# Kernel optimization log

Hardware: AMD Instinct MI355X
Metric: run time of the kernel (lower is better)

The kernel has to match this reference:

```python
import jax, jax.numpy as jnp
import numpy as np

# spconv.SparseConv4d(C_in, 16, (1,3,3,3), stride=1, padding=0) on spatial_shape [1000,1000,40]:
# leading kernel dim is size 1, so this is a regular (non-submanifold) 3D sparse conv,
# valid padding -> output spatial shape (998, 998, 38). Implemented as gather-GEMM-scatter:
# input point p contributes feat(p) @ W[k] to output coord p - offset[k] for each of 27 taps.

N = 200000
C_IN = 64
C_OUT = 16
K = 3
OUT_SP = (998, 998, 38)  # 1000-3+1, 1000-3+1, 40-3+1
SENT = OUT_SP[0] * OUT_SP[1] * OUT_SP[2]  # sentinel linear index for invalid taps


def setup_inputs() -> dict:
    key = jax.random.key(0)
    k1, k2, k3, k4, k5, k6 = jax.random.split(key, 6)
    feats = jax.random.normal(k1, (N, C_IN), dtype=jnp.float32)
    x = jax.random.randint(k2, (N,), 0, 1000, dtype=jnp.int32)
    y = jax.random.randint(k3, (N,), 0, 1000, dtype=jnp.int32)
    z = jax.random.randint(k4, (N,), 0, 40, dtype=jnp.int32)
    coords = jnp.stack([jnp.zeros((N,), jnp.int32), x, y, z], axis=1)  # [N,4] (b,x,y,z)
    fan_in = C_IN * K * K * K
    W = jax.random.normal(k5, (K * K * K, C_IN, C_OUT), dtype=jnp.float32) / np.sqrt(fan_in)
    bias = jax.random.normal(k6, (C_OUT,), dtype=jnp.float32) * 0.01
    return {"input": feats, "coords": coords, "W": W, "bias": bias}


def reference(input, coords, W, bias):
    # kernel tap offsets, C-order over (kx,ky,kz) in [0,3)^3 -> [27,3]
    off = jnp.stack(
        jnp.meshgrid(jnp.arange(K), jnp.arange(K), jnp.arange(K), indexing="ij"),
        axis=-1,
    ).reshape(K * K * K, 3).astype(jnp.int32)
    xyz = coords[:, 1:4]                              # [N,3]
    oc = xyz[:, None, :] - off[None, :, :]            # [N,27,3] output coord per tap
    out_sp = jnp.array(OUT_SP, dtype=jnp.int32)
    valid = jnp.all((oc >= 0) & (oc < out_sp), axis=-1)  # [N,27]
    lin = oc[..., 0] * (OUT_SP[1] * OUT_SP[2]) + oc[..., 1] * OUT_SP[2] + oc[..., 2]
    lin = jnp.where(valid, lin, SENT).reshape(-1)     # [N*27]

    # gather-GEMM: per-tap GEMM over all active voxels
    contrib = jnp.einsum("nc,kco->nko", input, W)     # [N,27,16]
    contrib = jnp.where(valid[..., None], contrib, 0.0).reshape(-1, C_OUT)

    NK = N * (K * K * K)
    uniq, inv = jnp.unique(lin, return_inverse=True, size=NK, fill_value=SENT)
    inv = inv.reshape(-1)
    # scatter-add into unique output sites
    out = jax.ops.segment_sum(contrib, inv, num_segments=NK)  # [NK,16]
    cnt = jax.ops.segment_sum(valid.reshape(-1).astype(jnp.int32), inv, num_segments=NK)
    out = out + jnp.where(cnt[:, None] > 0, bias[None, :], 0.0)
    return out, uniq
```

## Files before the change

### kernel.cpp

```cpp
#include <hip/hip_runtime.h>

#define N_PTS   200000
#define CIN     64
#define COUT    16
#define KK      27
#define SXD     998
#define SYD     998
#define SZD     38
#define STRX    (SYD*SZD)
#define SENTV   (SXD*SYD*SZD)
#define NKTOT   (N_PTS*KK)
#define NWORDS  ((SENTV+31)/32)
#define NCHUNK  ((NWORDS+255)/256)
#define NB      16000

typedef float f32x4 __attribute__((ext_vector_type(4)));

template<int S>
__global__ void mark_kernel(const int* __restrict__ coords, unsigned* __restrict__ bm,
                            unsigned* __restrict__ mu, unsigned* __restrict__ hist) {
    int n = blockIdx.x * blockDim.x + threadIdx.x;
    if (n >= N_PTS) return;
    int4 c = ((const int4*)coords)[n];
    int x = c.y, y = c.z, z = c.w;
    if (hist) {
        unsigned key = ((unsigned)x >> 3) * 128u + ((unsigned)y >> 3);
        atomicAdd(&hist[key], 1u);
    }
    int zlo = z - 2; if (zlo < 0) zlo = 0;
    int zhi = z;     if (zhi > SZD - 1) zhi = SZD - 1;
    unsigned nb = (unsigned)(zhi - zlo + 1);
    unsigned mseed = (1u << nb) - 1u;
    #pragma unroll
    for (int dx = 0; dx < 3; dx++) {
        int ox = x - dx;
        if (ox < 0 || ox >= SXD) continue;
        #pragma unroll
        for (int dy = 0; dy < 3; dy++) {
            int oy = y - dy;
            if (oy < 0 || oy >= SYD) continue;
            int lin = ox*STRX + oy*SZD + zlo;
            unsigned w = (unsigned)lin >> 5;
            unsigned b = (unsigned)lin & 31u;
            unsigned lowm = mseed << b;
            unsigned old = atomicOr(&bm[(size_t)w * S], lowm);
            unsigned col = old & lowm;
            if (col) atomicOr(&mu[(size_t)w * S], col);
            if (b + nb > 32u) {
                unsigned highm = mseed >> (32u - b);
                unsigned old2 = atomicOr(&bm[(size_t)(w+1) * S], highm);
                unsigned col2 = old2 & highm;
                if (col2) atomicOr(&mu[(size_t)(w+1) * S], col2);
            }
        }
    }
}

template<int S>
__global__ void chunk_sums_kernel(const unsigned* __restrict__ bm, unsigned* __restrict__ csums) {
    int w = blockIdx.x * 256 + threadIdx.x;
    unsigned c = (w < NWORDS) ? (unsigned)__popc(bm[(size_t)w * S]) : 0u;
    __shared__ unsigned s[256];
    s[threadIdx.x] = c;
    __syncthreads();
    for (int off = 128; off > 0; off >>= 1) {
        if (threadIdx.x < off) s[threadIdx.x] += s[threadIdx.x + off];
        __syncthreads();
    }
    if (threadIdx.x == 0) csums[blockIdx.x] = s[0];
}

__global__ void scan_all_kernel(const unsigned* __restrict__ csums,
                                unsigned* __restrict__ cprefix,
                                unsigned* __restrict__ Uptr,
                                const unsigned* __restrict__ hist,
                                unsigned* __restrict__ bpos,
                                int do_buckets) {
    __shared__ unsigned s[256];
    __shared__ unsigned run_s;
    if (threadIdx.x == 0) run_s = 0;
    __syncthreads();
    for (int base = 0; base < NCHUNK; base += 256) {
        int i = base + threadIdx.x;
        unsigned v = (i < NCHUNK) ? csums[i] : 0u;
        s[threadIdx.x] = v;
        __syncthreads();
        for (int off = 1; off < 256; off <<= 1) {
            unsigned t = (threadIdx.x >= off) ? s[threadIdx.x - off] : 0u;
            __syncthreads();
            s[threadIdx.x] += t;
            __syncthreads();
        }
        unsigned run = run_s;
        if (i < NCHUNK) cprefix[i] = run + s[threadIdx.x] - v;
        unsigned tile_total = s[255];
        __syncthreads();
        if (threadIdx.x == 255) run_s = run + tile_total;
        __syncthreads();
    }
    if (threadIdx.x == 0) Uptr[0] = run_s;
    if (!do_buckets) return;
    __syncthreads();
    if (threadIdx.x == 0) run_s = 0;
    __syncthreads();
    for (int base = 0; base < NB; base += 256) {
        int i = base + threadIdx.x;
        unsigned v = (i < NB) ? hist[i] : 0u;
        s[threadIdx.x] = v;
        __syncthreads();
        for (int off = 1; off < 256; off <<= 1) {
            unsigned t = (threadIdx.x >= off) ? s[threadIdx.x - off] : 0u;
            __syncthreads();
            s[threadIdx.x] += t;
            __syncthreads();
        }
        unsigned run = run_s;
        if (i < NB) bpos[i] = run + s[threadIdx.x] - v;
        unsigned tile_total = s[255];
        __syncthreads();
        if (threadIdx.x == 255) run_s = run + tile_total;
        __syncthreads();
    }
}

template<int S>
__global__ void word_prefix_kernel(const unsigned* __restrict__ bm,
                                   const unsigned* __restrict__ cprefix,
                                   unsigned* __restrict__ wp) {
    int w = blockIdx.x * 256 + threadIdx.x;
    unsigned v = (w < NWORDS) ? (unsigned)__popc(bm[(size_t)w * S]) : 0u;
    __shared__ unsigned s[256];
    s[threadIdx.x] = v;
    __syncthreads();
    for (int off = 1; off < 256; off <<= 1) {
        unsigned t = (threadIdx.x >= off) ? s[threadIdx.x - off] : 0u;
        __syncthreads();
        s[threadIdx.x] += t;
        __syncthreads();
    }
    if (w < NWORDS) wp[(size_t)w * S] = cprefix[blockIdx.x] + s[threadIdx.x] - v;
}

__global__ void pidx_kernel(const int* __restrict__ coords, unsigned* __restrict__ bpos,
                            int4* __restrict__ csorted) {
    int n = blockIdx.x * blockDim.x + threadIdx.x;
    if (n >= N_PTS) return;
    int4 c = ((const int4*)coords)[n];
    unsigned key = ((unsigned)c.y >> 3) * 128u + ((unsigned)c.z >> 3);
    unsigned pos = atomicAdd(&bpos[key], 1u);
    csorted[pos] = make_int4(n, c.y, c.z, c.w);
}

__global__ void fill_out_kernel(float* __restrict__ out, const float* __restrict__ bias,
                                const unsigned* __restrict__ Uptr) {
    unsigned U = Uptr[0];
    unsigned i = blockIdx.x * blockDim.x + threadIdx.x;
    if (i >= (unsigned)NKTOT * 4u) return;
    unsigned row = i >> 2;
    int q = i & 3;
    float4 v;
    if (row < U) v = ((const float4*)bias)[q];
    else         v = make_float4(0.f, 0.f, 0.f, 0.f);
    ((float4*)out)[i] = v;
}

__global__ void fill_uniq_kernel(float* __restrict__ uniq) {
    unsigned i = blockIdx.x * blockDim.x + threadIdx.x;
    if (i < (unsigned)NKTOT) uniq[i] = (float)SENTV;
}

__global__ void tail_kernel(float* __restrict__ out, float* __restrict__ uniq,
                            const unsigned* __restrict__ Uptr) {
    unsigned U = Uptr[0];
    unsigned i = blockIdx.x * blockDim.x + threadIdx.x;
    if (i >= (unsigned)NKTOT || i < U) return;
    f32x4 z4 = {0.f, 0.f, 0.f, 0.f};
    f32x4* dst = (f32x4*)(out + (size_t)i * COUT);
    #pragma unroll
    for (int q = 0; q < 4; q++) __builtin_nontemporal_store(z4, dst + q);
    __builtin_nontemporal_store((float)SENTV, uniq + i);
}

template<int S, bool DO_BIAS>
__global__ void write_uniq_kernel(const unsigned* __restrict__ bm,
                                  const unsigned* __restrict__ mu,
                                  const unsigned* __restrict__ wp,
                                  const unsigned* __restrict__ Uptr,
                                  float* __restrict__ uniq,
                                  float* __restrict__ out,
                                  const float* __restrict__ bias) {
    __shared__ float sbuf[8192];
    unsigned U = Uptr[0];
    int wfirst = blockIdx.x * 256;
    int wnext  = wfirst + 256;
    unsigned r0 = wp[(size_t)wfirst * S];
    unsigned r1 = (wnext < NWORDS) ? wp[(size_t)wnext * S] : U;
    int w = wfirst + threadIdx.x;
    unsigned bits = 0, r = 0, mbits = 0;
    if (w < NWORDS) {
        bits = bm[(size_t)w * S];
        r    = wp[(size_t)w * S];
        if (DO_BIAS) mbits = mu[(size_t)w * S];
    }
    unsigned bb = bits, rr = r;
    while (bb) {
        int b = __ffs(bb) - 1;
        bb &= bb - 1;
        sbuf[rr - r0] = (float)((unsigned)w * 32u + b);
        rr++;
    }
    __syncthreads();
    unsigned span = r1 - r0;
    for (unsigned j = threadIdx.x; j < span; j += 256)
        __builtin_nontemporal_store(sbuf[j], uniq + r0 + j);
    if (DO_BIAS && bits && mbits) {
        f32x4 bv[4];
        #pragma unroll
        for (int q = 0; q < 4; q++) bv[q] = ((const f32x4*)bias)[q];
        bb = bits; rr = r;
        while (bb) {
            int b = __ffs(bb) - 1;
            bb &= bb - 1;
            if ((mbits >> b) & 1u) {
                f32x4* dst = (f32x4*)(out + (size_t)rr * COUT);
                #pragma unroll
                for (int q = 0; q < 4; q++) __builtin_nontemporal_store(bv[q], dst + q);
            }
            rr++;
        }
    }
}

template<int S, bool SORTED>
__launch_bounds__(256)
__global__ void scatter_mm_kernel(const float* __restrict__ feats,
                                  const int4* __restrict__ cpts,
                                  const float* __restrict__ W,
                                  const float* __restrict__ bias,
                                  const unsigned* __restrict__ bm,
                                  const unsigned* __restrict__ mu,
                                  const unsigned* __restrict__ wp,
                                  float* __restrict__ out) {
    int i = blockIdx.x * 256 + threadIdx.x;
    if (i >= N_PTS) return;
    int dx = blockIdx.y;
    int4 cc = cpts[i];
    int n = SORTED ? cc.x : i;
    int x = cc.y, y = cc.z, z = cc.w;
    int ox = x - dx;
    if (ox < 0 || ox >= SXD) return;

    f32x4 f[CIN/4];
    const f32x4* fin4 = (const f32x4*)(feats + (size_t)n * CIN);
    #pragma unroll
    for (int q = 0; q < CIN/4; q++) f[q] = fin4[q];

    f32x4 bv[4];
    #pragma unroll
    for (int q = 0; q < 4; q++) bv[q] = ((const f32x4*)bias)[q];

    #pragma unroll 1
    for (int dy = 0; dy < 3; dy++) {
        int oy = y - dy;
        if (oy < 0 || oy >= SYD) continue;
        int colbase = ox*STRX + oy*SZD;
        #pragma unroll 1
        for (int dz = 0; dz < 3; dz++) {
            int oz = z - dz;
            if (oz < 0 || oz >= SZD) continue;
            int lin = colbase + oz;
            unsigned word = (unsigned)lin >> 5, bit = (unsigned)lin & 31u;
            unsigned rank;
            bool is_multi;
            if constexpr (S == 4) {
                uint4 md = ((const uint4*)bm)[word];
                rank = md.z + (unsigned)__popc(md.x & ((1u << bit) - 1u));
                is_multi = (md.y >> bit) & 1u;
            } else {
                rank = wp[word] + (unsigned)__popc(bm[word] & ((1u << bit) - 1u));
                is_multi = (mu[word] >> bit) & 1u;
            }

            int m = dx*9 + dy*3 + dz;
            const float* wk = W + (size_t)m * CIN * COUT;
            float acc[COUT];
            #pragma unroll
            for (int o = 0; o < COUT; o++) acc[o] = 0.f;
            #pragma unroll
            for (int c4 = 0; c4 < CIN/4; c4++) {
                f32x4 fv = f[c4];
                const float* wrow = wk + c4 * 4 * COUT;
                #pragma unroll
                for (int o = 0; o < COUT; o++) {
                    acc[o] += fv.x * wrow[o] + fv.y * wrow[COUT + o]
                            + fv.z * wrow[2*COUT + o] + fv.w * wrow[3*COUT + o];
                }
            }

            float* dst = out + (size_t)rank * COUT;
            if (!is_multi) {
                #pragma unroll
                for (int q = 0; q < 4; q++) {
                    f32x4 v;
                    v.x = acc[q*4+0] + bv[q].x;
                    v.y = acc[q*4+1] + bv[q].y;
                    v.z = acc[q*4+2] + bv[q].z;
                    v.w = acc[q*4+3] + bv[q].w;
                    ((f32x4*)dst)[q] = v;
                }
            } else {
                #pragma unroll
                for (int o = 0; o < COUT; o++) atomicAdd(dst + o, acc[o]);
            }
        }
    }
}

extern "C" void kernel_launch(void* const* d_in, const int* in_sizes, int n_in,
                              void* d_out, int out_size, void* d_ws, size_t ws_size,
                              hipStream_t stream) {
    const float* feats  = (const float*)d_in[0];
    const int*   coords = (const int*)d_in[1];
    const float* W      = (const float*)d_in[2];
    const float* bias   = (const float*)d_in[3];
    float* out  = (float*)d_out;
    float* uniq = out + (size_t)NKTOT * COUT;

    unsigned* ws = (unsigned*)d_ws;

    size_t o_meta    = 0;
    size_t o_hist    = o_meta + 4 * (size_t)NWORDS;
    size_t o_bpos    = o_hist + NB;
    size_t o_csums   = o_bpos + NB;
    size_t o_cprefix = o_csums + NCHUNK;
    size_t o_Uptr    = o_cprefix + NCHUNK;
    size_t o_csort   = (o_Uptr + 1 + 3) & ~(size_t)3;
    size_t fast_words = o_csort + 4 * (size_t)N_PTS;

    if (ws_size >= fast_words * sizeof(unsigned)) {
        unsigned* meta    = ws + o_meta;
        unsigned* hist    = ws + o_hist;
        unsigned* bpos    = ws + o_bpos;
        unsigned* csums   = ws + o_csums;
        unsigned* cprefix = ws + o_cprefix;
        unsigned* Uptr    = ws + o_Uptr;
        int4*     csorted = (int4*)(ws + o_csort);

        hipMemsetAsync(meta, 0, (4 * (size_t)NWORDS + NB) * sizeof(unsigned), stream);
        mark_kernel<4><<<(N_PTS + 255) / 256, 256, 0, stream>>>(coords, meta, meta + 1, hist);
        chunk_sums_kernel<4><<<NCHUNK, 256, 0, stream>>>(meta, csums);
        scan_all_kernel<<<1, 256, 0, stream>>>(csums, cprefix, Uptr, hist, bpos, 1);
        pidx_kernel<<<(N_PTS + 255) / 256, 256, 0, stream>>>(coords, bpos, csorted);
        word_prefix_kernel<4><<<NCHUNK, 256, 0, stream>>>(meta, cprefix, meta + 2);
        write_uniq_kernel<4, true><<<NCHUNK, 256, 0, stream>>>(
            meta, meta + 1, meta + 2, Uptr, uniq, out, bias);
        tail_kernel<<<(NKTOT + 255) / 256, 256, 0, stream>>>(out, uniq, Uptr);
        scatter_mm_kernel<4, true><<<dim3((N_PTS + 255) / 256, 3), 256, 0, stream>>>(
            feats, csorted, W, bias, meta, meta + 1, meta + 2, out);
    } else {
        unsigned* bitmap  = ws;
        unsigned* wprefix = ws + NWORDS;
        unsigned* csums   = ws + 2 * (size_t)NWORDS;
        unsigned* cprefix = csums + NCHUNK;
        unsigned* Uptr    = cprefix + NCHUNK;

        hipMemsetAsync(bitmap, 0, (size_t)NWORDS * sizeof(unsigned), stream);
        mark_kernel<1><<<(N_PTS + 255) / 256, 256, 0, stream>>>(coords, bitmap, bitmap, nullptr);
        chunk_sums_kernel<1><<<NCHUNK, 256, 0, stream>>>(bitmap, csums);
        scan_all_kernel<<<1, 256, 0, stream>>>(csums, cprefix, Uptr, nullptr, nullptr, 0);
        word_prefix_kernel<1><<<NCHUNK, 256, 0, stream>>>(bitmap, cprefix, wprefix);
        fill_out_kernel<<<(NKTOT * 4 + 255) / 256, 256, 0, stream>>>(out, bias, Uptr);
        fill_uniq_kernel<<<(NKTOT + 255) / 256, 256, 0, stream>>>(uniq);
        write_uniq_kernel<1, false><<<NCHUNK, 256, 0, stream>>>(
            bitmap, bitmap, wprefix, Uptr, uniq, out, bias);
        scatter_mm_kernel<1, false><<<dim3((N_PTS + 255) / 256, 3), 256, 0, stream>>>(
            feats, (const int4*)coords, W, bias, bitmap, bitmap, wprefix, out);
    }
}
```

Before: 1.251 ms.

## Split interleaved metadata into separate arrays and fuse dx taps into one thread

Replaces the stride-4 interleaved bitmap/multi/prefix layout with separate contiguous arrays. Each scatter thread now handles all three dx offsets instead of one per blockIdx.y, preloading the nine column metadata words and computing the ranks of consecutive z voxels as r0+j. Feature loads and coordinate reads are therefore shared across 27 taps, and metadata lookups drop to about nine per point. The two prefix scans now run in parallel across two blocks. The cost is higher register pressure and fewer threads in the scatter kernel, which lowers parallelism.

```diff
diff --git a/kernel.cpp b/kernel.cpp
--- a/kernel.cpp
+++ b/kernel.cpp
@@ -16,7 +16,6 @@
 
 typedef float f32x4 __attribute__((ext_vector_type(4)));
 
-template<int S>
 __global__ void mark_kernel(const int* __restrict__ coords, unsigned* __restrict__ bm,
                             unsigned* __restrict__ mu, unsigned* __restrict__ hist) {
     int n = blockIdx.x * blockDim.x + threadIdx.x;
@@ -43,23 +42,22 @@
             unsigned w = (unsigned)lin >> 5;
             unsigned b = (unsigned)lin & 31u;
             unsigned lowm = mseed << b;
-            unsigned old = atomicOr(&bm[(size_t)w * S], lowm);
+            unsigned old = atomicOr(&bm[w], lowm);
             unsigned col = old & lowm;
-            if (col) atomicOr(&mu[(size_t)w * S], col);
+            if (col) atomicOr(&mu[w], col);
             if (b + nb > 32u) {
                 unsigned highm = mseed >> (32u - b);
-                unsigned old2 = atomicOr(&bm[(size_t)(w+1) * S], highm);
+                unsigned old2 = atomicOr(&bm[w+1], highm);
                 unsigned col2 = old2 & highm;
-                if (col2) atomicOr(&mu[(size_t)(w+1) * S], col2);
+                if (col2) atomicOr(&mu[w+1], col2);
             }
         }
     }
 }
 
-template<int S>
 __global__ void chunk_sums_kernel(const unsigned* __restrict__ bm, unsigned* __restrict__ csums) {
     int w = blockIdx.x * 256 + threadIdx.x;
-    unsigned c = (w < NWORDS) ? (unsigned)__popc(bm[(size_t)w * S]) : 0u;
+    unsigned c = (w < NWORDS) ? (unsigned)__popc(bm[w]) : 0u;
     __shared__ unsigned s[256];
     s[threadIdx.x] = c;
     __syncthreads();
@@ -78,11 +76,15 @@
                                 int do_buckets) {
     __shared__ unsigned s[256];
     __shared__ unsigned run_s;
+    if (blockIdx.x == 1 && !do_buckets) return;
+    const unsigned* src = (blockIdx.x == 0) ? csums : hist;
+    unsigned* dst       = (blockIdx.x == 0) ? cprefix : bpos;
+    int count           = (blockIdx.x == 0) ? NCHUNK : NB;
     if (threadIdx.x == 0) run_s = 0;
     __syncthreads();
-    for (int base = 0; base < NCHUNK; base += 256) {
+    for (int base = 0; base < count; base += 256) {
         int i = base + threadIdx.x;
-        unsigned v = (i < NCHUNK) ? csums[i] : 0u;
+        unsigned v = (i < count) ? src[i] : 0u;
         s[threadIdx.x] = v;
         __syncthreads();
         for (int off = 1; off < 256; off <<= 1) {
@@ -92,43 +94,20 @@
             __syncthreads();
         }
         unsigned run = run_s;
-        if (i < NCHUNK) cprefix[i] = run + s[threadIdx.x] - v;
+        if (i < count) dst[i] = run + s[threadIdx.x] - v;
         unsigned tile_total = s[255];
         __syncthreads();
         if (threadIdx.x == 255) run_s = run + tile_total;
         __syncthreads();
     }
-    if (threadIdx.x == 0) Uptr[0] = run_s;
-    if (!do_buckets) return;
-    __syncthreads();
-    if (threadIdx.x == 0) run_s = 0;
-    __syncthreads();
-    for (int base = 0; base < NB; base += 256) {
-        int i = base + threadIdx.x;
-        unsigned v = (i < NB) ? hist[i] : 0u;
-        s[threadIdx.x] = v;
-        __syncthreads();
-        for (int off = 1; off < 256; off <<= 1) {
-            unsigned t = (threadIdx.x >= off) ? s[threadIdx.x - off] : 0u;
-            __syncthreads();
-            s[threadIdx.x] += t;
-            __syncthreads();
-        }
-        unsigned run = run_s;
-        if (i < NB) bpos[i] = run + s[threadIdx.x] - v;
-        unsigned tile_total = s[255];
-        __syncthreads();
-        if (threadIdx.x == 255) run_s = run + tile_total;
-        __syncthreads();
-    }
-}
-
-template<int S>
+    if (blockIdx.x == 0 && threadIdx.x == 0) Uptr[0] = run_s;
+}
+
 __global__ void word_prefix_kernel(const unsigned* __restrict__ bm,
                                    const unsigned* __restrict__ cprefix,
                                    unsigned* __restrict__ wp) {
     int w = blockIdx.x * 256 + threadIdx.x;
-    unsigned v = (w < NWORDS) ? (unsigned)__popc(bm[(size_t)w * S]) : 0u;
+    unsigned v = (w < NWORDS) ? (unsigned)__popc(bm[w]) : 0u;
     __shared__ unsigned s[256];
     s[threadIdx.x] = v;
     __syncthreads();
@@ -138,7 +117,7 @@
         s[threadIdx.x] += t;
         __syncthreads();
     }
-    if (w < NWORDS) wp[(size_t)w * S] = cprefix[blockIdx.x] + s[threadIdx.x] - v;
+    if (w < NWORDS) wp[w] = cprefix[blockIdx.x] + s[threadIdx.x] - v;
 }
 
 __global__ void pidx_kernel(const int* __restrict__ coords, unsigned* __restrict__ bpos,
@@ -181,7 +160,7 @@
     __builtin_nontemporal_store((float)SENTV, uniq + i);
 }
 
-template<int S, bool DO_BIAS>
+template<bool DO_BIAS>
 __global__ void write_uniq_kernel(const unsigned* __restrict__ bm,
                                   const unsigned* __restrict__ mu,
                                   const unsigned* __restrict__ wp,
@@ -193,14 +172,14 @@
     unsigned U = Uptr[0];
     int wfirst = blockIdx.x * 256;
     int wnext  = wfirst + 256;
-    unsigned r0 = wp[(size_t)wfirst * S];
-    unsigned r1 = (wnext < NWORDS) ? wp[(size_t)wnext * S] : U;
+    unsigned r0 = wp[wfirst];
+    unsigned r1 = (wnext < NWORDS) ? wp[wnext] : U;
     int w = wfirst + threadIdx.x;
     unsigned bits = 0, r = 0, mbits = 0;
     if (w < NWORDS) {
-        bits = bm[(size_t)w * S];
-        r    = wp[(size_t)w * S];
-        if (DO_BIAS) mbits = mu[(size_t)w * S];
+        bits = bm[w];
+        r    = wp[w];
+        if (DO_BIAS) mbits = mu[w];
     }
     unsigned bb = bits, rr = r;
     while (bb) {
@@ -231,7 +210,7 @@
     }
 }
 
-template<int S, bool SORTED>
+template<bool SORTED>
 __launch_bounds__(256)
 __global__ void scatter_mm_kernel(const float* __restrict__ feats,
                                   const int4* __restrict__ cpts,
@@ -243,12 +222,32 @@
                                   float* __restrict__ out) {
     int i = blockIdx.x * 256 + threadIdx.x;
     if (i >= N_PTS) return;
-    int dx = blockIdx.y;
     int4 cc = cpts[i];
     int n = SORTED ? cc.x : i;
     int x = cc.y, y = cc.z, z = cc.w;
-    int ox = x - dx;
-    if (ox < 0 || ox >= SXD) return;
+
+    int zlo = z - 2; if (zlo < 0) zlo = 0;
+
+    unsigned bmv[9], muv[9], mu2v[9], wpv[9], b0v[9];
+    bool valv[9];
+    #pragma unroll
+    for (int dx = 0; dx < 3; dx++) {
+        int ox = x - dx;
+        #pragma unroll
+        for (int dy = 0; dy < 3; dy++) {
+            int k = dx*3 + dy;
+            int oy = y - dy;
+            bool v = (ox >= 0) & (ox < SXD) & (oy >= 0) & (oy < SYD);
+            valv[k] = v;
+            unsigned lin0 = (unsigned)(ox*STRX + oy*SZD + zlo);
+            unsigned w0 = v ? (lin0 >> 5) : 0u;
+            b0v[k] = lin0 & 31u;
+            bmv[k]  = v ? bm[w0] : 0u;
+            muv[k]  = v ? mu[w0] : 0u;
+            mu2v[k] = (v && (lin0 & 31u) >= 30u) ? mu[w0 + 1] : 0u;
+            wpv[k]  = v ? wp[w0] : 0u;
+        }
+    }
 
     f32x4 f[CIN/4];
     const f32x4* fin4 = (const f32x4*)(feats + (size_t)n * CIN);
@@ -260,57 +259,53 @@
     for (int q = 0; q < 4; q++) bv[q] = ((const f32x4*)bias)[q];
 
     #pragma unroll 1
-    for (int dy = 0; dy < 3; dy++) {
-        int oy = y - dy;
-        if (oy < 0 || oy >= SYD) continue;
-        int colbase = ox*STRX + oy*SZD;
+    for (int dx = 0; dx < 3; dx++) {
         #pragma unroll 1
-        for (int dz = 0; dz < 3; dz++) {
-            int oz = z - dz;
-            if (oz < 0 || oz >= SZD) continue;
-            int lin = colbase + oz;
-            unsigned word = (unsigned)lin >> 5, bit = (unsigned)lin & 31u;
-            unsigned rank;
-            bool is_multi;
-            if constexpr (S == 4) {
-                uint4 md = ((const uint4*)bm)[word];
-                rank = md.z + (unsigned)__popc(md.x & ((1u << bit) - 1u));
-                is_multi = (md.y >> bit) & 1u;
-            } else {
-                rank = wp[word] + (unsigned)__popc(bm[word] & ((1u << bit) - 1u));
-                is_multi = (mu[word] >> bit) & 1u;
-            }
-
-            int m = dx*9 + dy*3 + dz;
-            const float* wk = W + (size_t)m * CIN * COUT;
-            float acc[COUT];
+        for (int dy = 0; dy < 3; dy++) {
+            int k = dx*3 + dy;
+            if (!valv[k]) continue;
+            unsigned b0 = b0v[k];
+            unsigned r0 = wpv[k] + (unsigned)__popc(bmv[k] & ((1u << b0) - 1u));
+            unsigned mlo = muv[k], mhi = mu2v[k];
             #pragma unroll
-            for (int o = 0; o < COUT; o++) acc[o] = 0.f;
-            #pragma unroll
-            for (int c4 = 0; c4 < CIN/4; c4++) {
-                f32x4 fv = f[c4];
-                const float* wrow = wk + c4 * 4 * COUT;
+            for (int dz = 0; dz < 3; dz++) {
+                int oz = z - dz;
+                if (oz < 0 || oz >= SZD) continue;
+                unsigned j = (unsigned)(oz - zlo);
+                unsigned bb = b0 + j;
+                bool ismul = (((bb < 32u) ? (mlo >> bb) : (mhi >> (bb - 32u))) & 1u) != 0u;
+                unsigned rank = r0 + j;
+
+                const float* wk = W + (size_t)(dx*9 + dy*3 + dz) * (CIN*COUT);
+                float acc[COUT];
                 #pragma unroll
-                for (int o = 0; o < COUT; o++) {
-                    acc[o] += fv.x * wrow[o] + fv.y * wrow[COUT + o]
-                            + fv.z * wrow[2*COUT + o] + fv.w * wrow[3*COUT + o];
+                for (int o = 0; o < COUT; o++) acc[o] = 0.f;
+                #pragma unroll
+                for (int c4 = 0; c4 < CIN/4; c4++) {
+                    f32x4 fv = f[c4];
+                    const float* wrow = wk + c4 * 4 * COUT;
+                    #pragma unroll
+                    for (int o = 0; o < COUT; o++) {
+                        acc[o] += fv.x * wrow[o] + fv.y * wrow[COUT + o]
+                                + fv.z * wrow[2*COUT + o] + fv.w * wrow[3*COUT + o];
+                    }
                 }
-            }
-
-            float* dst = out + (size_t)rank * COUT;
-            if (!is_multi) {
-                #pragma unroll
-                for (int q = 0; q < 4; q++) {
-                    f32x4 v;
-                    v.x = acc[q*4+0] + bv[q].x;
-                    v.y = acc[q*4+1] + bv[q].y;
-                    v.z = acc[q*4+2] + bv[q].z;
-                    v.w = acc[q*4+3] + bv[q].w;
-                    ((f32x4*)dst)[q] = v;
+
+                float* dst = out + (size_t)rank * COUT;
+                if (!ismul) {
+                    #pragma unroll
+                    for (int q = 0; q < 4; q++) {
+                        f32x4 vv;
+                        vv.x = acc[q*4+0] + bv[q].x;
+                        vv.y = acc[q*4+1] + bv[q].y;
+                        vv.z = acc[q*4+2] + bv[q].z;
+                        vv.w = acc[q*4+3] + bv[q].w;
+                        ((f32x4*)dst)[q] = vv;
+                    }
+                } else {
+                    #pragma unroll
+                    for (int o = 0; o < COUT; o++) atomicAdd(dst + o, acc[o]);
                 }
-            } else {
-                #pragma unroll
-                for (int o = 0; o < COUT; o++) atomicAdd(dst + o, acc[o]);
             }
         }
     }
@@ -328,9 +323,11 @@
 
     unsigned* ws = (unsigned*)d_ws;
 
-    size_t o_meta    = 0;
-    size_t o_hist    = o_meta + 4 * (size_t)NWORDS;
-    size_t o_bpos    = o_hist + NB;
+    size_t o_bm      = 0;
+    size_t o_mu      = o_bm + NWORDS;
+    size_t o_hist    = o_mu + NWORDS;
+    size_t o_wp      = o_hist + NB;
+    size_t o_bpos    = o_wp + NWORDS;
     size_t o_csums   = o_bpos + NB;
     size_t o_cprefix = o_csums + NCHUNK;
     size_t o_Uptr    = o_cprefix + NCHUNK;
@@ -338,42 +335,44 @@
     size_t fast_words = o_csort + 4 * (size_t)N_PTS;
 
     if (ws_size >= fast_words * sizeof(unsigned)) {
-        unsigned* meta    = ws + o_meta;
+        unsigned* bm      = ws + o_bm;
+        unsigned* mu      = ws + o_mu;
         unsigned* hist    = ws + o_hist;
+        unsigned* wp      = ws + o_wp;
         unsigned* bpos    = ws + o_bpos;
         unsigned* csums   = ws + o_csums;
         unsigned* cprefix = ws + o_cprefix;
         unsigned* Uptr    = ws + o_Uptr;
         int4*     csorted = (int4*)(ws + o_csort);
 
-        hipMemsetAsync(meta, 0, (4 * (size_t)NWORDS + NB) * sizeof(unsigned), stream);
-        mark_kernel<4><<<(N_PTS + 255) / 256, 256, 0, stream>>>(coords, meta, meta + 1, hist);
-        chunk_sums_kernel<4><<<NCHUNK, 256, 0, stream>>>(meta, csums);
-        scan_all_kernel<<<1, 256, 0, stream>>>(csums, cprefix, Uptr, hist, bpos, 1);
+        hipMemsetAsync(bm, 0, (2 * (size_t)NWORDS + NB) * sizeof(unsigned), stream);
+        mark_kernel<<<(N_PTS + 255) / 256, 256, 0, stream>>>(coords, bm, mu, hist);
+        chunk_sums_kernel<<<NCHUNK, 256, 0, stream>>>(bm, csums);
+        scan_all_kernel<<<2, 256, 0, stream>>>(csums, cprefix, Uptr, hist, bpos, 1);
         pidx_kernel<<<(N_PTS + 255) / 256, 256, 0, stream>>>(coords, bpos, csorted);
-        word_prefix_kernel<4><<<NCHUNK, 256, 0, stream>>>(meta, cprefix, meta + 2);
-        write_uniq_kernel<4, true><<<NCHUNK, 256, 0, stream>>>(
-            meta, meta + 1, meta + 2, Uptr, uniq, out, bias);
+        word_prefix_kernel<<<NCHUNK, 256, 0, stream>>>(bm, cprefix, wp);
+        write_uniq_kernel<true><<<NCHUNK, 256, 0, stream>>>(
+            bm, mu, wp, Uptr, uniq, out, bias);
         tail_kernel<<<(NKTOT + 255) / 256, 256, 0, stream>>>(out, uniq, Uptr);
-        scatter_mm_kernel<4, true><<<dim3((N_PTS + 255) / 256, 3), 256, 0, stream>>>(
-            feats, csorted, W, bias, meta, meta + 1, meta + 2, out);
+        scatter_mm_kernel<true><<<(N_PTS + 255) / 256, 256, 0, stream>>>(
+            feats, csorted, W, bias, bm, mu, wp, out);
     } else {
-        unsigned* bitmap  = ws;
-        unsigned* wprefix = ws + NWORDS;
+        unsigned* bm      = ws;
+        unsigned* wp      = ws + NWORDS;
         unsigned* csums   = ws + 2 * (size_t)NWORDS;
         unsigned* cprefix = csums + NCHUNK;
         unsigned* Uptr    = cprefix + NCHUNK;
 
-        hipMemsetAsync(bitmap, 0, (size_t)NWORDS * sizeof(unsigned), stream);
-        mark_kernel<1><<<(N_PTS + 255) / 256, 256, 0, stream>>>(coords, bitmap, bitmap, nullptr);
-        chunk_sums_kernel<1><<<NCHUNK, 256, 0, stream>>>(bitmap, csums);
-        scan_all_kernel<<<1, 256, 0, stream>>>(csums, cprefix, Uptr, nullptr, nullptr, 0);
-        word_prefix_kernel<1><<<NCHUNK, 256, 0, stream>>>(bitmap, cprefix, wprefix);
+        hipMemsetAsync(bm, 0, (size_t)NWORDS * sizeof(unsigned), stream);
+        mark_kernel<<<(N_PTS + 255) / 256, 256, 0, stream>>>(coords, bm, bm, nullptr);
+        chunk_sums_kernel<<<NCHUNK, 256, 0, stream>>>(bm, csums);
+        scan_all_kernel<<<2, 256, 0, stream>>>(csums, cprefix, Uptr, nullptr, nullptr, 0);
+        word_prefix_kernel<<<NCHUNK, 256, 0, stream>>>(bm, cprefix, wp);
         fill_out_kernel<<<(NKTOT * 4 + 255) / 256, 256, 0, stream>>>(out, bias, Uptr);
         fill_uniq_kernel<<<(NKTOT + 255) / 256, 256, 0, stream>>>(uniq);
-        write_uniq_kernel<1, false><<<NCHUNK, 256, 0, stream>>>(
-            bitmap, bitmap, wprefix, Uptr, uniq, out, bias);
-        scatter_mm_kernel<1, false><<<dim3((N_PTS + 255) / 256, 3), 256, 0, stream>>>(
-            feats, (const int4*)coords, W, bias, bitmap, bitmap, wprefix, out);
-    }
-}
+        write_uniq_kernel<false><<<NCHUNK, 256, 0, stream>>>(
+            bm, bm, wp, Uptr, uniq, out, bias);
+        scatter_mm_kernel<false><<<(N_PTS + 255) / 256, 256, 0, stream>>>(
+            feats, (const int4*)coords, W, bias, bm, bm, wp, out);
+    }
+}
```

After: 1.472 ms. +17.7%, slower.
